# Performance work log

Hardware: AMD Instinct MI355X
Metric: run time of the kernel (lower is better)

## Reference

```python
import jax, jax.numpy as jnp
import numpy as np

N = 8192       # nodes
E = 131072     # edges
R = 4          # relations
IN_EMBD = 64   # per-feature embedding dim -> node feat = 6*64 = 384
H1 = 256       # layer_embd
D = 128        # out_embd; layer2 outputs 2*D
VOCABS = [35, 10, 5, 7, 5, 5]


def setup_inputs() -> dict:
    key = jax.random.key(0)
    ks = jax.random.split(key, 20)
    inp = {}
    inp['x'] = jax.random.randint(ks[0], (N, 6), 0, 5)
    inp['edge_index'] = jax.random.randint(ks[1], (2, E), 0, N)
    inp['edge_type'] = jax.random.randint(ks[2], (E,), 0, R)
    for i, v in enumerate(VOCABS):
        inp[f'emb{i}'] = jax.random.normal(ks[3 + i], (v, IN_EMBD), jnp.float32) * 0.1
    inp['W1'] = jax.random.normal(ks[10], (R, 6 * IN_EMBD, H1), jnp.float32) * 0.05
    inp['root1'] = jax.random.normal(ks[11], (6 * IN_EMBD, H1), jnp.float32) * 0.05
    inp['b1'] = jnp.zeros((H1,), jnp.float32)
    inp['W2'] = jax.random.normal(ks[12], (R, H1, 2 * D), jnp.float32) * 0.05
    inp['root2'] = jax.random.normal(ks[13], (H1, 2 * D), jnp.float32) * 0.05
    inp['b2'] = jnp.zeros((2 * D,), jnp.float32)
    return inp


def _rgcn(h, W, root, b, src, dst, edge_type):
    # RGCNConv (PyG semantics): out_i = root h_i + b + sum_r mean_{j in N_r(i)} W_r h_j
    out = h @ root + b
    for r in range(R):
        hr = h @ W[r]                                   # [N, out]
        m = (edge_type == r).astype(h.dtype)            # [E]
        s = jax.ops.segment_sum(hr[src] * m[:, None], dst, num_segments=N)
        c = jax.ops.segment_sum(m, dst, num_segments=N)
        out = out + s / jnp.clip(c, 1.0)[:, None]
    return out


def reference(x, edge_index, edge_type, emb0, emb1, emb2, emb3, emb4, emb5,
              W1, root1, b1, W2, root2, b2):
    embs = [emb0, emb1, emb2, emb3, emb4, emb5]
    x_ = jnp.concatenate([embs[i][x[:, i]] for i in range(6)], axis=1)  # [N, 384]
    src, dst = edge_index[0], edge_index[1]
    h1 = jax.nn.sigmoid(_rgcn(x_, W1, root1, b1, src, dst, edge_type))
    h2 = jax.nn.sigmoid(_rgcn(h1, W2, root2, b2, src, dst, edge_type))
    mu, logvar = h2[:, :D], h2[:, D:]
    std = jnp.exp(0.5 * logvar)
    eps = jax.random.normal(jax.random.key(42), std.shape, std.dtype)
    Z = eps * std + mu                                   # reparametrize
    A_hat = jax.nn.sigmoid(Z @ Z.T)                      # [N, N]
    A = jnp.zeros((N, N), jnp.float32).at[src, dst].set(1.0)
    return A, A_hat, mu, logvar
```

## Files before the change

kernel.cpp:

```cpp
#include <hip/hip_runtime.h>
#include <hip/hip_bf16.h>
#include <cstdint>
#include <cstddef>

#define N_NODES 8192
#define NE      131072
#define NR      4
#define NC      1280
#define SLOTS   96

typedef __attribute__((ext_vector_type(8))) short bf16x8;
typedef __attribute__((ext_vector_type(4))) float f32x4;

__device__ __forceinline__ float sigmoidf_(float x) {
  return 1.0f / (1.0f + __expf(-x));
}

__device__ __forceinline__ ushort f2b(float v) {
  __hip_bfloat16 h = __float2bfloat16(v);
  return *(ushort*)&h;
}
__device__ __forceinline__ float b2f(ushort u) {
  __hip_bfloat16 h = *(__hip_bfloat16*)&u;
  return __bfloat162float(h);
}
__device__ __forceinline__ void split2(float v, ushort& hi, ushort& lo) {
  hi = f2b(v);
  lo = f2b(v - b2f(hi));
}

__global__ void k_embed(const int* __restrict__ xi,
                        const float* __restrict__ e0, const float* __restrict__ e1,
                        const float* __restrict__ e2, const float* __restrict__ e3,
                        const float* __restrict__ e4, const float* __restrict__ e5,
                        ushort* __restrict__ xhi) {
  int n = blockIdx.x;
  int c = threadIdx.x;
  int i = c >> 6, d = c & 63;
  const float* t;
  switch (i) {
    case 0: t = e0; break; case 1: t = e1; break; case 2: t = e2; break;
    case 3: t = e3; break; case 4: t = e4; break; default: t = e5; break;
  }
  float v = t[(size_t)xi[n * 6 + i] * 64 + d];
  xhi[(size_t)n * 384 + c] = f2b(v);
}

__global__ __launch_bounds__(256) void k_pack_all(
    const float* __restrict__ r1, const float* __restrict__ W1,
    const float* __restrict__ r2, const float* __restrict__ W2,
    ushort* __restrict__ B1t, ushort* __restrict__ B2thi, ushort* __restrict__ B2tlo) {
  __shared__ ushort sh[64][66];
  __shared__ ushort sl[64][66];
  int b = blockIdx.x;
  int layer, K, kt, nt, seg;
  const float *srcR, *srcW;
  if (b < 120) { layer = 1; K = 384; int t = b;       seg = t / 24; t %= 24; kt = t / 4; nt = t % 4; srcR = r1; srcW = W1; }
  else         { layer = 2; K = 256; int t = b - 120; seg = t / 16; t %= 16; kt = t / 4; nt = t % 4; srcR = r2; srcW = W2; }
  int k0 = kt * 64, n0 = nt * 64;
  int tid = threadIdx.x;
#pragma unroll
  for (int it = 0; it < 16; ++it) {
    int idx = it * 256 + tid;
    int kl = idx >> 6, nl = idx & 63;
    int kg = k0 + kl, c = n0 + nl;
    float v = (seg == 0) ? srcR[(size_t)kg * 256 + c]
                         : srcW[((size_t)(seg - 1) * K + kg) * 256 + c];
    ushort h, l; split2(v, h, l);
    sh[kl][nl] = h;
    sl[kl][nl] = l;
  }
  __syncthreads();
#pragma unroll
  for (int it = 0; it < 16; ++it) {
    int idx = it * 256 + tid;
    int nl = idx >> 6, kl = idx & 63;
    size_t o = (size_t)(seg * 256 + n0 + nl) * K + k0 + kl;
    if (layer == 1) {
      B1t[o] = sh[kl][nl];
    } else {
      B2thi[o] = sh[kl][nl];
      B2tlo[o] = sl[kl][nl];
    }
  }
}

__global__ void k_zero_i(int* __restrict__ p, int n) {
  int i = blockIdx.x * 256 + threadIdx.x;
  if (i < n) p[i] = 0;
}
__global__ void k_fill_slots(const int* __restrict__ src, const int* __restrict__ dst,
                             const int* __restrict__ et,
                             int* __restrict__ cnt, int* __restrict__ slots) {
  int e = blockIdx.x * 256 + threadIdx.x;
  if (e < NE) {
    int d = dst[e];
    int pos = atomicAdd(&cnt[d], 1);
    if (pos < SLOTS) slots[(size_t)d * SLOTS + pos] = (src[e] << 2) | et[e];
  }
}

template<int SPLIT3, int ACT, int SYM>
__global__ __launch_bounds__(256) void k_gemm2(
    const ushort* __restrict__ Ahi, const ushort* __restrict__ Alo,
    const ushort* __restrict__ Bhi, const ushort* __restrict__ Blo,
    float* __restrict__ C, int Nc, int K) {
  __shared__ ushort Bs[(SPLIT3 ? 2 : 1) * 128 * 128];
  ushort* BsH = Bs;
  ushort* BsL = Bs + 128 * 128;

  const int tid = threadIdx.x;
  const int w = tid >> 6, l = tid & 63;
  const int lrow = l & 15, lk8 = (l >> 4) * 8;

  int brow, bcol, p = 0, q = 0;
  if (SYM) {
    int b = blockIdx.x;
    q = (int)((sqrtf(8.f * (float)b + 1.f) - 1.f) * 0.5f);
    while ((q + 1) * (q + 2) / 2 <= b) ++q;
    while (q * (q + 1) / 2 > b) --q;
    p = b - q * (q + 1) / 2;
    brow = p * 128; bcol = q * 128;
  } else {
    brow = blockIdx.y * 128; bcol = blockIdx.x * 128;
  }

  f32x4 acc[2][8] = {};
  const size_t arow0 = (size_t)(brow + w * 32 + lrow) * K + lk8;
  const size_t arow1 = arow0 + (size_t)16 * K;

  for (int kc = 0; kc < K; kc += 128) {
    bf16x8 aH[4][2], aL[4][2];
#pragma unroll
    for (int kk = 0; kk < 4; ++kk) {
      aH[kk][0] = *(const bf16x8*)(Ahi + arow0 + kc + kk * 32);
      aH[kk][1] = *(const bf16x8*)(Ahi + arow1 + kc + kk * 32);
      if (SPLIT3) {
        aL[kk][0] = *(const bf16x8*)(Alo + arow0 + kc + kk * 32);
        aL[kk][1] = *(const bf16x8*)(Alo + arow1 + kc + kk * 32);
      }
    }
    if (kc) __syncthreads();
#pragma unroll
    for (int it = 0; it < 8; ++it) {
      int o = (it * 256 + tid) * 16;
      int row = o >> 8, sb = o & 255;
      int se = (sb ^ ((row & 7) << 4)) >> 1;
      size_t g = (size_t)(bcol + row) * K + kc + se;
      *(uint4*)((char*)BsH + o) = *(const uint4*)(Bhi + g);
      if (SPLIT3) *(uint4*)((char*)BsL + o) = *(const uint4*)(Blo + g);
    }
    __syncthreads();
#pragma unroll
    for (int kk = 0; kk < 4; ++kk) {
#pragma unroll
      for (int n = 0; n < 8; ++n) {
        int row_t = n * 16 + lrow;
        int addr = row_t * 256 + ((kk * 64 + (l >> 4) * 16) ^ ((row_t & 7) << 4));
        bf16x8 b_h = *(const bf16x8*)((const char*)BsH + addr);
        acc[0][n] = __builtin_amdgcn_mfma_f32_16x16x32_bf16(aH[kk][0], b_h, acc[0][n], 0, 0, 0);
        acc[1][n] = __builtin_amdgcn_mfma_f32_16x16x32_bf16(aH[kk][1], b_h, acc[1][n], 0, 0, 0);
        if (SPLIT3) {
          bf16x8 b_l = *(const bf16x8*)((const char*)BsL + addr);
          acc[0][n] = __builtin_amdgcn_mfma_f32_16x16x32_bf16(aL[kk][0], b_h, acc[0][n], 0, 0, 0);
          acc[1][n] = __builtin_amdgcn_mfma_f32_16x16x32_bf16(aL[kk][1], b_h, acc[1][n], 0, 0, 0);
          acc[0][n] = __builtin_amdgcn_mfma_f32_16x16x32_bf16(aH[kk][0], b_l, acc[0][n], 0, 0, 0);
          acc[1][n] = __builtin_amdgcn_mfma_f32_16x16x32_bf16(aH[kk][1], b_l, acc[1][n], 0, 0, 0);
        }
      }
    }
  }

  const int crow = (l >> 4) * 4, ccol = l & 15;
#pragma unroll
  for (int m = 0; m < 2; ++m)
#pragma unroll
    for (int n = 0; n < 8; ++n) {
      float v[4];
#pragma unroll
      for (int r = 0; r < 4; ++r) {
        float t = acc[m][n][r];
        v[r] = ACT ? sigmoidf_(t) : t;
      }
      int rloc = w * 32 + m * 16 + crow;
      int cloc = n * 16 + ccol;
      float* cp = C + (size_t)(brow + rloc) * Nc + bcol + cloc;
#pragma unroll
      for (int r = 0; r < 4; ++r) cp[(size_t)r * Nc] = v[r];
      if (SYM && p != q) {
        float* mp = C + (size_t)(bcol + cloc) * Nc + brow + rloc;
        *(float4*)mp = make_float4(v[0], v[1], v[2], v[3]);
      }
    }
}

__device__ __forceinline__ float bits_to_normal(unsigned bits) {
  float f = __uint_as_float((bits >> 9) | 0x3f800000u) - 1.0f;
  const float lo = -0.99999994f;
  float u = __fadd_rn(__fmul_rn(f, 2.0f), lo);
  u = fmaxf(lo, u);
  float w = -log1pf(-u * u);
  float p;
  if (w < 5.0f) {
    w = w - 2.5f;
    p = 2.81022636e-08f;
    p = fmaf(p, w, 3.43273939e-07f);
    p = fmaf(p, w, -3.5233877e-06f);
    p = fmaf(p, w, -4.39150654e-06f);
    p = fmaf(p, w, 0.00021858087f);
    p = fmaf(p, w, -0.00125372503f);
    p = fmaf(p, w, -0.00417768164f);
    p = fmaf(p, w, 0.246640727f);
    p = fmaf(p, w, 1.50140941f);
  } else {
    w = sqrtf(w) - 3.0f;
    p = -0.000200214257f;
    p = fmaf(p, w, 0.000100950558f);
    p = fmaf(p, w, 0.00134934322f);
    p = fmaf(p, w, -0.00367342844f);
    p = fmaf(p, w, 0.00573950773f);
    p = fmaf(p, w, -0.0076224613f);
    p = fmaf(p, w, 0.00943887047f);
    p = fmaf(p, w, 1.00167406f);
    p = fmaf(p, w, 2.83297682f);
  }
  return 1.41421356f * (p * u);
}

__device__ __forceinline__ unsigned threefry_bits(unsigned j) {
  const unsigned ks0 = 0u, ks1 = 42u, ks2 = 0x1BD11BDAu ^ 0u ^ 42u;
  unsigned x0 = 0u + ks0;
  unsigned x1 = j + ks1;
#define RND(r) { x0 += x1; x1 = (x1 << r) | (x1 >> (32 - r)); x1 ^= x0; }
  RND(13) RND(15) RND(26) RND(6)  x0 += ks1; x1 += ks2 + 1u;
  RND(17) RND(29) RND(16) RND(24) x0 += ks2; x1 += ks0 + 2u;
  RND(13) RND(15) RND(26) RND(6)  x0 += ks0; x1 += ks1 + 3u;
  RND(17) RND(29) RND(16) RND(24) x0 += ks1; x1 += ks2 + 4u;
  RND(13) RND(15) RND(26) RND(6)  x0 += ks2; x1 += ks0 + 5u;
#undef RND
  return x0 ^ x1;
}

__global__ __launch_bounds__(256) void k_combine1(
    const float* __restrict__ hall, const float* __restrict__ bias,
    const int* __restrict__ cnt, const int* __restrict__ slots,
    ushort* __restrict__ h_hi, ushort* __restrict__ h_lo) {
  __shared__ int sc[64];
  int n = blockIdx.x, c = threadIdx.x;
  int end = min(cnt[n], SLOTS);
  const int* sl = slots + (size_t)n * SLOTS;
  float a0 = 0.f, a1 = 0.f, a2 = 0.f, a3 = 0.f;
  int c0 = 0, c1 = 0, c2 = 0, c3 = 0;
  for (int base = 0; base < end; base += 64) {
    int mcnt = min(64, end - base);
    if (c < 64 && base + c < end) sc[c] = sl[base + c];
    __syncthreads();
    int i = 0;
    for (; i + 4 <= mcnt; i += 4) {
      int p0 = sc[i], p1 = sc[i + 1], p2 = sc[i + 2], p3 = sc[i + 3];
      float v0 = hall[(size_t)(p0 >> 2) * NC + 256 + (size_t)(p0 & 3) * 256 + c];
      float v1 = hall[(size_t)(p1 >> 2) * NC + 256 + (size_t)(p1 & 3) * 256 + c];
      float v2 = hall[(size_t)(p2 >> 2) * NC + 256 + (size_t)(p2 & 3) * 256 + c];
      float v3 = hall[(size_t)(p3 >> 2) * NC + 256 + (size_t)(p3 & 3) * 256 + c];
      int r;
      r = p0 & 3; if (r == 0) { a0 += v0; ++c0; } else if (r == 1) { a1 += v0; ++c1; }
                  else if (r == 2) { a2 += v0; ++c2; } else { a3 += v0; ++c3; }
      r = p1 & 3; if (r == 0) { a0 += v1; ++c0; } else if (r == 1) { a1 += v1; ++c1; }
                  else if (r == 2) { a2 += v1; ++c2; } else { a3 += v1; ++c3; }
      r = p2 & 3; if (r == 0) { a0 += v2; ++c0; } else if (r == 1) { a1 += v2; ++c1; }
                  else if (r == 2) { a2 += v2; ++c2; } else { a3 += v2; ++c3; }
      r = p3 & 3; if (r == 0) { a0 += v3; ++c0; } else if (r == 1) { a1 += v3; ++c1; }
                  else if (r == 2) { a2 += v3; ++c2; } else { a3 += v3; ++c3; }
    }
    for (; i < mcnt; ++i) {
      int pp = sc[i];
      int r = pp & 3;
      float v = hall[(size_t)(pp >> 2) * NC + 256 + (size_t)r * 256 + c];
      if (r == 0) { a0 += v; ++c0; } else if (r == 1) { a1 += v; ++c1; }
      else if (r == 2) { a2 += v; ++c2; } else { a3 += v; ++c3; }
    }
    __syncthreads();
  }
  float v = hall[(size_t)n * NC + c] + bias[c]
          + a0 / (float)max(c0, 1) + a1 / (float)max(c1, 1)
          + a2 / (float)max(c2, 1) + a3 / (float)max(c3, 1);
  float sg = sigmoidf_(v);
  ushort h, l; split2(sg, h, l);
  h_hi[(size_t)n * 256 + c] = h;
  h_lo[(size_t)n * 256 + c] = l;
}

__global__ __launch_bounds__(256) void k_combine2z(
    const float* __restrict__ hall, const float* __restrict__ bias,
    const int* __restrict__ cnt, const int* __restrict__ slots,
    float* __restrict__ muo, float* __restrict__ lvo,
    ushort* __restrict__ zhi, ushort* __restrict__ zlo) {
  __shared__ int sc[64];
  __shared__ float sv[256];
  int n = blockIdx.x, c = threadIdx.x;
  int end = min(cnt[n], SLOTS);
  const int* sl = slots + (size_t)n * SLOTS;
  float a0 = 0.f, a1 = 0.f, a2 = 0.f, a3 = 0.f;
  int c0 = 0, c1 = 0, c2 = 0, c3 = 0;
  for (int base = 0; base < end; base += 64) {
    int mcnt = min(64, end - base);
    if (c < 64 && base + c < end) sc[c] = sl[base + c];
    __syncthreads();
    int i = 0;
    for (; i + 4 <= mcnt; i += 4) {
      int p0 = sc[i], p1 = sc[i + 1], p2 = sc[i + 2], p3 = sc[i + 3];
      float v0 = hall[(size_t)(p0 >> 2) * NC + 256 + (size_t)(p0 & 3) * 256 + c];
      float v1 = hall[(size_t)(p1 >> 2) * NC + 256 + (size_t)(p1 & 3) * 256 + c];
      float v2 = hall[(size_t)(p2 >> 2) * NC + 256 + (size_t)(p2 & 3) * 256 + c];
      float v3 = hall[(size_t)(p3 >> 2) * NC + 256 + (size_t)(p3 & 3) * 256 + c];
      int r;
      r = p0 & 3; if (r == 0) { a0 += v0; ++c0; } else if (r == 1) { a1 += v0; ++c1; }
                  else if (r == 2) { a2 += v0; ++c2; } else { a3 += v0; ++c3; }
      r = p1 & 3; if (r == 0) { a0 += v1; ++c0; } else if (r == 1) { a1 += v1; ++c1; }
                  else if (r == 2) { a2 += v1; ++c2; } else { a3 += v1; ++c3; }
      r = p2 & 3; if (r == 0) { a0 += v2; ++c0; } else if (r == 1) { a1 += v2; ++c1; }
                  else if (r == 2) { a2 += v2; ++c2; } else { a3 += v2; ++c3; }
      r = p3 & 3; if (r == 0) { a0 += v3; ++c0; } else if (r == 1) { a1 += v3; ++c1; }
                  else if (r == 2) { a2 += v3; ++c2; } else { a3 += v3; ++c3; }
    }
    for (; i < mcnt; ++i) {
      int pp = sc[i];
      int r = pp & 3;
      float v = hall[(size_t)(pp >> 2) * NC + 256 + (size_t)r * 256 + c];
      if (r == 0) { a0 += v; ++c0; } else if (r == 1) { a1 += v; ++c1; }
      else if (r == 2) { a2 += v; ++c2; } else { a3 += v; ++c3; }
    }
    __syncthreads();
  }
  float v = hall[(size_t)n * NC + c] + bias[c]
          + a0 / (float)max(c0, 1) + a1 / (float)max(c1, 1)
          + a2 / (float)max(c2, 1) + a3 / (float)max(c3, 1);
  float sg = sigmoidf_(v);
  if (c < 128) muo[(size_t)n * 128 + c] = sg;
  else         lvo[(size_t)n * 128 + (c - 128)] = sg;
  sv[c] = sg;
  __syncthreads();
  if (c < 128) {
    unsigned j = (unsigned)n * 128u + (unsigned)c;
    float e = bits_to_normal(threefry_bits(j));
    float z = fmaf(e, __expf(0.5f * sv[c + 128]), sv[c]);
    ushort h, l; split2(z, h, l);
    zhi[j] = h; zlo[j] = l;
  }
}

__global__ void k_zerof4(float4* __restrict__ p, size_t n4) {
  size_t i = (size_t)blockIdx.x * blockDim.x + threadIdx.x;
  size_t stride = (size_t)gridDim.x * blockDim.x;
  float4 z = make_float4(0.f, 0.f, 0.f, 0.f);
  for (; i < n4; i += stride) p[i] = z;
}

__global__ void k_scatterA(const int* __restrict__ src, const int* __restrict__ dst,
                           float* __restrict__ A) {
  int e = blockIdx.x * 256 + threadIdx.x;
  if (e < NE) A[(size_t)src[e] * N_NODES + dst[e]] = 1.0f;
}

extern "C" void kernel_launch(void* const* d_in, const int* in_sizes, int n_in,
                              void* d_out, int out_size, void* d_ws, size_t ws_size,
                              hipStream_t stream) {
  const int* x    = (const int*)d_in[0];
  const int* ei   = (const int*)d_in[1];
  const int* src  = ei;
  const int* dst  = ei + NE;
  const int* et   = (const int*)d_in[2];
  const float* e0 = (const float*)d_in[3];
  const float* e1 = (const float*)d_in[4];
  const float* e2 = (const float*)d_in[5];
  const float* e3 = (const float*)d_in[6];
  const float* e4 = (const float*)d_in[7];
  const float* e5 = (const float*)d_in[8];
  const float* W1 = (const float*)d_in[9];
  const float* r1 = (const float*)d_in[10];
  const float* b1 = (const float*)d_in[11];
  const float* W2 = (const float*)d_in[12];
  const float* r2 = (const float*)d_in[13];
  const float* b2 = (const float*)d_in[14];

  float* out  = (float*)d_out;
  float* A    = out;
  float* Ahat = out + (size_t)N_NODES * N_NODES;
  float* muo  = Ahat + (size_t)N_NODES * N_NODES;
  float* lvo  = muo + (size_t)N_NODES * 128;

  char* wp = (char*)d_ws;
  auto carve = [&](size_t bytes) { char* r = wp; wp += (bytes + 255) & ~(size_t)255; return r; };
  ushort* xhi   = (ushort*)carve((size_t)8192 * 384 * 2);
  ushort* B1t   = (ushort*)carve((size_t)NC * 384 * 2);
  ushort* B2thi = (ushort*)carve((size_t)NC * 256 * 2);
  ushort* B2tlo = (ushort*)carve((size_t)NC * 256 * 2);
  float*  hall  = (float*)carve((size_t)8192 * NC * 4);
  ushort* h1hi  = (ushort*)carve((size_t)8192 * 256 * 2);
  ushort* h1lo  = (ushort*)carve((size_t)8192 * 256 * 2);
  ushort* zhi   = (ushort*)carve((size_t)8192 * 128 * 2);
  ushort* zlo   = (ushort*)carve((size_t)8192 * 128 * 2);
  int*    cnt   = (int*)carve((size_t)8192 * 4);
  int*    slots = (int*)carve((size_t)8192 * SLOTS * 4);

  k_zero_i<<<32, 256, 0, stream>>>(cnt, 8192);
  k_fill_slots<<<NE / 256, 256, 0, stream>>>(src, dst, et, cnt, slots);

  k_embed<<<8192, 384, 0, stream>>>(x, e0, e1, e2, e3, e4, e5, xhi);
  k_pack_all<<<200, 256, 0, stream>>>(r1, W1, r2, W2, B1t, B2thi, B2tlo);

  k_gemm2<0, 0, 0><<<dim3(NC / 128, 64), 256, 0, stream>>>(
      xhi, nullptr, B1t, nullptr, hall, NC, 384);
  k_combine1<<<8192, 256, 0, stream>>>(hall, b1, cnt, slots, h1hi, h1lo);

  k_gemm2<1, 0, 0><<<dim3(NC / 128, 64), 256, 0, stream>>>(
      h1hi, h1lo, B2thi, B2tlo, hall, NC, 256);
  k_combine2z<<<8192, 256, 0, stream>>>(hall, b2, cnt, slots, muo, lvo, zhi, zlo);

  k_zerof4<<<8192, 256, 0, stream>>>((float4*)A, (size_t)N_NODES * N_NODES / 4);
  k_scatterA<<<NE / 256, 256, 0, stream>>>(src, dst, A);

  k_gemm2<1, 1, 1><<<dim3(64 * 65 / 2), 256, 0, stream>>>(
      zhi, zlo, zhi, zlo, Ahat, N_NODES, 128);
}
```

Baseline: 340.1 us.

## Stage mirrored Ahat tile through LDS, store layer-1 hall as bf16, fuse scatter

```diff
diff --git a/kernel.cpp b/kernel.cpp
--- a/kernel.cpp
+++ b/kernel.cpp
@@ -85,26 +85,24 @@
   }
 }
 
-__global__ void k_zero_i(int* __restrict__ p, int n) {
-  int i = blockIdx.x * 256 + threadIdx.x;
-  if (i < n) p[i] = 0;
-}
-__global__ void k_fill_slots(const int* __restrict__ src, const int* __restrict__ dst,
-                             const int* __restrict__ et,
-                             int* __restrict__ cnt, int* __restrict__ slots) {
+__global__ void k_fill_scatter(const int* __restrict__ src, const int* __restrict__ dst,
+                               const int* __restrict__ et,
+                               int* __restrict__ cnt, int* __restrict__ slots,
+                               float* __restrict__ A) {
   int e = blockIdx.x * 256 + threadIdx.x;
   if (e < NE) {
-    int d = dst[e];
+    int d = dst[e], s = src[e];
     int pos = atomicAdd(&cnt[d], 1);
-    if (pos < SLOTS) slots[(size_t)d * SLOTS + pos] = (src[e] << 2) | et[e];
-  }
-}
-
-template<int SPLIT3, int ACT, int SYM>
+    if (pos < SLOTS) slots[(size_t)d * SLOTS + pos] = (s << 2) | et[e];
+    A[(size_t)s * N_NODES + d] = 1.0f;
+  }
+}
+
+template<int SPLIT3, int ACT, int SYM, int OUT>
 __global__ __launch_bounds__(256) void k_gemm2(
     const ushort* __restrict__ Ahi, const ushort* __restrict__ Alo,
     const ushort* __restrict__ Bhi, const ushort* __restrict__ Blo,
-    float* __restrict__ C, int Nc, int K) {
+    void* __restrict__ Cv, int Nc, int K) {
   __shared__ ushort Bs[(SPLIT3 ? 2 : 1) * 128 * 128];
   ushort* BsH = Bs;
   ushort* BsL = Bs + 128 * 128;
@@ -172,6 +170,11 @@
   }
 
   const int crow = (l >> 4) * 4, ccol = l & 15;
+  float*  Cf = (float*)Cv;
+  ushort* Cb = (ushort*)Cv;
+  const int domirror = (SYM && p != q);
+  if (SYM) { if (domirror) __syncthreads(); }
+  float* T = (float*)Bs;
 #pragma unroll
   for (int m = 0; m < 2; ++m)
 #pragma unroll
@@ -184,14 +187,29 @@
       }
       int rloc = w * 32 + m * 16 + crow;
       int cloc = n * 16 + ccol;
-      float* cp = C + (size_t)(brow + rloc) * Nc + bcol + cloc;
-#pragma unroll
-      for (int r = 0; r < 4; ++r) cp[(size_t)r * Nc] = v[r];
+#pragma unroll
+      for (int r = 0; r < 4; ++r) {
+        if (OUT) Cb[(size_t)(brow + rloc + r) * Nc + bcol + cloc] = f2b(v[r]);
+        else     Cf[(size_t)(brow + rloc + r) * Nc + bcol + cloc] = v[r];
+      }
       if (SYM && p != q) {
-        float* mp = C + (size_t)(bcol + cloc) * Nc + brow + rloc;
-        *(float4*)mp = make_float4(v[0], v[1], v[2], v[3]);
+        int s = (cloc & 7) << 2;
+#pragma unroll
+        for (int r = 0; r < 4; ++r) T[cloc * 128 + ((rloc + r) ^ s)] = v[r];
       }
     }
+  if (SYM && p != q) {
+    __syncthreads();
+#pragma unroll
+    for (int it = 0; it < 16; ++it) {
+      int idx = it * 256 + tid;
+      int rw = idx >> 5;
+      int c4 = (idx & 31) * 4;
+      int s = (rw & 7) << 2;
+      float4 val = *(const float4*)&T[rw * 128 + (c4 ^ s)];
+      *(float4*)(Cf + (size_t)(bcol + rw) * Nc + brow + c4) = val;
+    }
+  }
 }
 
 __device__ __forceinline__ float bits_to_normal(unsigned bits) {
@@ -242,10 +260,61 @@
 }
 
 __global__ __launch_bounds__(256) void k_combine1(
-    const float* __restrict__ hall, const float* __restrict__ bias,
+    const ushort* __restrict__ hall, const float* __restrict__ bias,
     const int* __restrict__ cnt, const int* __restrict__ slots,
     ushort* __restrict__ h_hi, ushort* __restrict__ h_lo) {
   __shared__ int sc[64];
+  int n = blockIdx.x, c = threadIdx.x;
+  int end = min(cnt[n], SLOTS);
+  const int* sl = slots + (size_t)n * SLOTS;
+  float a0 = 0.f, a1 = 0.f, a2 = 0.f, a3 = 0.f;
+  int c0 = 0, c1 = 0, c2 = 0, c3 = 0;
+  for (int base = 0; base < end; base += 64) {
+    int mcnt = min(64, end - base);
+    if (c < 64 && base + c < end) sc[c] = sl[base + c];
+    __syncthreads();
+    int i = 0;
+    for (; i + 4 <= mcnt; i += 4) {
+      int p0 = sc[i], p1 = sc[i + 1], p2 = sc[i + 2], p3 = sc[i + 3];
+      float v0 = b2f(hall[(size_t)(p0 >> 2) * NC + 256 + (size_t)(p0 & 3) * 256 + c]);
+      float v1 = b2f(hall[(size_t)(p1 >> 2) * NC + 256 + (size_t)(p1 & 3) * 256 + c]);
+      float v2 = b2f(hall[(size_t)(p2 >> 2) * NC + 256 + (size_t)(p2 & 3) * 256 + c]);
+      float v3 = b2f(hall[(size_t)(p3 >> 2) * NC + 256 + (size_t)(p3 & 3) * 256 + c]);
+      int r;
+      r = p0 & 3; if (r == 0) { a0 += v0; ++c0; } else if (r == 1) { a1 += v0; ++c1; }
+                  else if (r == 2) { a2 += v0; ++c2; } else { a3 += v0; ++c3; }
+      r = p1 & 3; if (r == 0) { a0 += v1; ++c0; } else if (r == 1) { a1 += v1; ++c1; }
+                  else if (r == 2) { a2 += v1; ++c2; } else { a3 += v1; ++c3; }
+      r = p2 & 3; if (r == 0) { a0 += v2; ++c0; } else if (r == 1) { a1 += v2; ++c1; }
+                  else if (r == 2) { a2 += v2; ++c2; } else { a3 += v2; ++c3; }
+      r = p3 & 3; if (r == 0) { a0 += v3; ++c0; } else if (r == 1) { a1 += v3; ++c1; }
+                  else if (r == 2) { a2 += v3; ++c2; } else { a3 += v3; ++c3; }
+    }
+    for (; i < mcnt; ++i) {
+      int pp = sc[i];
+      int r = pp & 3;
+      float v = b2f(hall[(size_t)(pp >> 2) * NC + 256 + (size_t)r * 256 + c]);
+      if (r == 0) { a0 += v; ++c0; } else if (r == 1) { a1 += v; ++c1; }
+      else if (r == 2) { a2 += v; ++c2; } else { a3 += v; ++c3; }
+    }
+    __syncthreads();
+  }
+  float v = b2f(hall[(size_t)n * NC + c]) + bias[c]
+          + a0 / (float)max(c0, 1) + a1 / (float)max(c1, 1)
+          + a2 / (float)max(c2, 1) + a3 / (float)max(c3, 1);
+  float sg = sigmoidf_(v);
+  ushort h, l; split2(sg, h, l);
+  h_hi[(size_t)n * 256 + c] = h;
+  h_lo[(size_t)n * 256 + c] = l;
+}
+
+__global__ __launch_bounds__(256) void k_combine2z(
+    const float* __restrict__ hall, const float* __restrict__ bias,
+    const int* __restrict__ cnt, const int* __restrict__ slots,
+    float* __restrict__ muo, float* __restrict__ lvo,
+    ushort* __restrict__ zhi, ushort* __restrict__ zlo) {
+  __shared__ int sc[64];
+  __shared__ float sv[256];
   int n = blockIdx.x, c = threadIdx.x;
   int end = min(cnt[n], SLOTS);
   const int* sl = slots + (size_t)n * SLOTS;
@@ -285,57 +354,6 @@
           + a0 / (float)max(c0, 1) + a1 / (float)max(c1, 1)
           + a2 / (float)max(c2, 1) + a3 / (float)max(c3, 1);
   float sg = sigmoidf_(v);
-  ushort h, l; split2(sg, h, l);
-  h_hi[(size_t)n * 256 + c] = h;
-  h_lo[(size_t)n * 256 + c] = l;
-}
-
-__global__ __launch_bounds__(256) void k_combine2z(
-    const float* __restrict__ hall, const float* __restrict__ bias,
-    const int* __restrict__ cnt, const int* __restrict__ slots,
-    float* __restrict__ muo, float* __restrict__ lvo,
-    ushort* __restrict__ zhi, ushort* __restrict__ zlo) {
-  __shared__ int sc[64];
-  __shared__ float sv[256];
-  int n = blockIdx.x, c = threadIdx.x;
-  int end = min(cnt[n], SLOTS);
-  const int* sl = slots + (size_t)n * SLOTS;
-  float a0 = 0.f, a1 = 0.f, a2 = 0.f, a3 = 0.f;
-  int c0 = 0, c1 = 0, c2 = 0, c3 = 0;
-  for (int base = 0; base < end; base += 64) {
-    int mcnt = min(64, end - base);
-    if (c < 64 && base + c < end) sc[c] = sl[base + c];
-    __syncthreads();
-    int i = 0;
-    for (; i + 4 <= mcnt; i += 4) {
-      int p0 = sc[i], p1 = sc[i + 1], p2 = sc[i + 2], p3 = sc[i + 3];
-      float v0 = hall[(size_t)(p0 >> 2) * NC + 256 + (size_t)(p0 & 3) * 256 + c];
-      float v1 = hall[(size_t)(p1 >> 2) * NC + 256 + (size_t)(p1 & 3) * 256 + c];
-      float v2 = hall[(size_t)(p2 >> 2) * NC + 256 + (size_t)(p2 & 3) * 256 + c];
-      float v3 = hall[(size_t)(p3 >> 2) * NC + 256 + (size_t)(p3 & 3) * 256 + c];
-      int r;
-      r = p0 & 3; if (r == 0) { a0 += v0; ++c0; } else if (r == 1) { a1 += v0; ++c1; }
-                  else if (r == 2) { a2 += v0; ++c2; } else { a3 += v0; ++c3; }
-      r = p1 & 3; if (r == 0) { a0 += v1; ++c0; } else if (r == 1) { a1 += v1; ++c1; }
-                  else if (r == 2) { a2 += v1; ++c2; } else { a3 += v1; ++c3; }
-      r = p2 & 3; if (r == 0) { a0 += v2; ++c0; } else if (r == 1) { a1 += v2; ++c1; }
-                  else if (r == 2) { a2 += v2; ++c2; } else { a3 += v2; ++c3; }
-      r = p3 & 3; if (r == 0) { a0 += v3; ++c0; } else if (r == 1) { a1 += v3; ++c1; }
-                  else if (r == 2) { a2 += v3; ++c2; } else { a3 += v3; ++c3; }
-    }
-    for (; i < mcnt; ++i) {
-      int pp = sc[i];
-      int r = pp & 3;
-      float v = hall[(size_t)(pp >> 2) * NC + 256 + (size_t)r * 256 + c];
-      if (r == 0) { a0 += v; ++c0; } else if (r == 1) { a1 += v; ++c1; }
-      else if (r == 2) { a2 += v; ++c2; } else { a3 += v; ++c3; }
-    }
-    __syncthreads();
-  }
-  float v = hall[(size_t)n * NC + c] + bias[c]
-          + a0 / (float)max(c0, 1) + a1 / (float)max(c1, 1)
-          + a2 / (float)max(c2, 1) + a3 / (float)max(c3, 1);
-  float sg = sigmoidf_(v);
   if (c < 128) muo[(size_t)n * 128 + c] = sg;
   else         lvo[(size_t)n * 128 + (c - 128)] = sg;
   sv[c] = sg;
@@ -354,12 +372,6 @@
   size_t stride = (size_t)gridDim.x * blockDim.x;
   float4 z = make_float4(0.f, 0.f, 0.f, 0.f);
   for (; i < n4; i += stride) p[i] = z;
-}
-
-__global__ void k_scatterA(const int* __restrict__ src, const int* __restrict__ dst,
-                           float* __restrict__ A) {
-  int e = blockIdx.x * 256 + threadIdx.x;
-  if (e < NE) A[(size_t)src[e] * N_NODES + dst[e]] = 1.0f;
 }
 
 extern "C" void kernel_launch(void* const* d_in, const int* in_sizes, int n_in,
@@ -396,6 +408,7 @@
   ushort* B2thi = (ushort*)carve((size_t)NC * 256 * 2);
   ushort* B2tlo = (ushort*)carve((size_t)NC * 256 * 2);
   float*  hall  = (float*)carve((size_t)8192 * NC * 4);
+  ushort* hallb = (ushort*)hall;
   ushort* h1hi  = (ushort*)carve((size_t)8192 * 256 * 2);
   ushort* h1lo  = (ushort*)carve((size_t)8192 * 256 * 2);
   ushort* zhi   = (ushort*)carve((size_t)8192 * 128 * 2);
@@ -403,23 +416,21 @@
   int*    cnt   = (int*)carve((size_t)8192 * 4);
   int*    slots = (int*)carve((size_t)8192 * SLOTS * 4);
 
-  k_zero_i<<<32, 256, 0, stream>>>(cnt, 8192);
-  k_fill_slots<<<NE / 256, 256, 0, stream>>>(src, dst, et, cnt, slots);
+  k_zerof4<<<8192, 256, 0, stream>>>((float4*)A, (size_t)N_NODES * N_NODES / 4);
+  hipMemsetAsync(cnt, 0, (size_t)8192 * 4, stream);
+  k_fill_scatter<<<NE / 256, 256, 0, stream>>>(src, dst, et, cnt, slots, A);
 
   k_embed<<<8192, 384, 0, stream>>>(x, e0, e1, e2, e3, e4, e5, xhi);
   k_pack_all<<<200, 256, 0, stream>>>(r1, W1, r2, W2, B1t, B2thi, B2tlo);
 
-  k_gemm2<0, 0, 0><<<dim3(NC / 128, 64), 256, 0, stream>>>(
-      xhi, nullptr, B1t, nullptr, hall, NC, 384);
-  k_combine1<<<8192, 256, 0, stream>>>(hall, b1, cnt, slots, h1hi, h1lo);
-
-  k_gemm2<1, 0, 0><<<dim3(NC / 128, 64), 256, 0, stream>>>(
+  k_gemm2<0, 0, 0, 1><<<dim3(NC / 128, 64), 256, 0, stream>>>(
+      xhi, nullptr, B1t, nullptr, hallb, NC, 384);
+  k_combine1<<<8192, 256, 0, stream>>>(hallb, b1, cnt, slots, h1hi, h1lo);
+
+  k_gemm2<1, 0, 0, 0><<<dim3(NC / 128, 64), 256, 0, stream>>>(
       h1hi, h1lo, B2thi, B2tlo, hall, NC, 256);
   k_combine2z<<<8192, 256, 0, stream>>>(hall, b2, cnt, slots, muo, lvo, zhi, zlo);
 
-  k_zerof4<<<8192, 256, 0, stream>>>((float4*)A, (size_t)N_NODES * N_NODES / 4);
-  k_scatterA<<<NE / 256, 256, 0, stream>>>(src, dst, A);
-
-  k_gemm2<1, 1, 1><<<dim3(64 * 65 / 2), 256, 0, stream>>>(
+  k_gemm2<1, 1, 1, 0><<<dim3(64 * 65 / 2), 256, 0, stream>>>(
       zhi, zlo, zhi, zlo, Ahat, N_NODES, 128);
 }
```

Result: faster. 291.1 us (-14.4%).
